# Optimization experiments

Measured on AMD Instinct MI355X. Metric: run time of the kernel, lower is better.

The kernel has to match this reference:

```python
import jax, jax.numpy as jnp
import numpy as np

B, NCAP, LV, LT, C = 64, 64, 197, 32, 512
NSP = LV - 1          # 196 spatial patches
NUM_KEEP = 98         # ceil(196 * sparse_ratio=0.5)
KEEPED = 49           # int(196 * aggr_ratio=0.5 * sparse_ratio=0.5)
HID = 102             # int(512 * dim_ratio=0.2)
LN_EPS = 1e-5


def _normalize(x):
    # torch F.normalize: x / max(||x||, 1e-12)
    return x / jnp.maximum(jnp.linalg.norm(x, axis=-1, keepdims=True), 1e-12)


def setup_inputs() -> dict:
    key = jax.random.key(0)
    ks = jax.random.split(key, 8)
    def rn(k, shape, s=0.02):
        return jax.random.normal(k, shape, jnp.float32) * s
    return {
        "img_embs": jax.random.normal(ks[0], (B, LV, C), jnp.float32),
        "cap_embs": jax.random.normal(ks[1], (NCAP, LT, C), jnp.float32),
        "cap_lens": jnp.full((NCAP,), LT, jnp.int32),
        "ln_gamma": jnp.ones((C,), jnp.float32),
        "ln_beta": jnp.zeros((C,), jnp.float32),
        "w1": rn(ks[2], (C, HID)), "b1": jnp.zeros((HID,), jnp.float32),
        "w2": rn(ks[3], (HID, KEEPED)), "b2": jnp.zeros((KEEPED,), jnp.float32),
        "aggr_scale": jnp.ones((1, 1, 1), jnp.float32),
        "wi2t": rn(ks[4], (C, C)), "bi2t": jnp.zeros((C,), jnp.float32),
        "wt2i": rn(ks[5], (C, C)), "bt2i": jnp.zeros((C,), jnp.float32),
        "temp": jnp.ones((1, 1, 1), jnp.float32),
    }


def _forward(img_embs, cap_embs, ln_gamma, ln_beta, w1, b1, w2, b2,
             aggr_scale, wi2t, bi2t, wt2i, bt2i, temp):
    img_norm = _normalize(img_embs)
    img_cls = img_embs[:, 0:1]              # [B,1,C]  has_cls_token branch
    img_sp = img_embs[:, 1:]                # [B,196,C]
    img_sp_norm = img_norm[:, 1:]
    # use_cls_as_glob_embd: global = normalized CLS (no grad)
    glo = jax.lax.stop_gradient(img_norm[:, 0:1])
    attn_x = jax.lax.stop_gradient(jnp.sum(glo * img_sp_norm, -1))  # [B,196]
    cap_norm = _normalize(cap_embs)
    bidx = jnp.arange(B)[:, None]

    def ln(x):
        m = x.mean(-1, keepdims=True)
        v = jnp.var(x, axis=-1, keepdims=True)
        return (x - m) / jnp.sqrt(v + LN_EPS) * ln_gamma + ln_beta

    def per_caption(cap_i, cap_i_norm):
        # cap_i, cap_i_norm: [LT, C]
        cap_glo = jax.lax.stop_gradient(_normalize(cap_i[0:1]))           # [1,C]
        attn_y = jax.lax.stop_gradient(jnp.sum(cap_glo[None] * img_sp_norm, -1))  # [B,196]
        # --- TokenSparse ---
        score = attn_x + attn_y
        order = jnp.argsort(-score, axis=1)                              # descending
        keep, nonkeep = order[:, :NUM_KEEP], order[:, NUM_KEEP:]
        sel = img_sp[bidx, keep]                                          # [B,98,C]
        non = img_sp[bidx, nonkeep]                                       # [B,98,C]
        non_score = jnp.take_along_axis(score, nonkeep, 1)
        extra = jnp.sum(non * jax.nn.softmax(non_score, axis=1)[..., None],
                        axis=1, keepdims=True)                            # [B,1,C]
        # --- TokenAggregation ---
        h = jax.nn.gelu(ln(sel) @ w1 + b1, approximate=False)             # [B,98,HID]
        w = jnp.swapaxes(h @ w2 + b2, 1, 2) * aggr_scale                  # [B,49,98]
        aggr = jax.nn.softmax(w, axis=2) @ sel                            # [B,49,C]
        # [cls, aggr, extra] -> [B,51,C], then normalize
        sel_tok = _normalize(jnp.concatenate([img_cls, aggr, extra], 1))
        Ls = sel_tok.shape[1]
        # --- 'attn' similarity ---
        cap_exp = jnp.broadcast_to(cap_i_norm[None], (B, LT, C))
        st = jnp.swapaxes(sel_tok, 1, 2)                                  # [B,C,51]
        c2i = jax.nn.leaky_relu(cap_exp @ st, negative_slope=0.1)         # [B,LT,51]
        a_i2t = jax.nn.softmax((cap_exp @ wi2t + bi2t) @ st / temp, axis=1)
        a_t2i = jax.nn.softmax((cap_exp @ wt2i + bt2i) @ st / temp, axis=2)
        return jnp.sum(a_i2t * c2i / Ls + a_t2i * c2i / LT, axis=(1, 2))  # [B]

    sims = jax.vmap(per_caption)(cap_embs, cap_norm)                      # [NCAP,B]
    return sims.T                                                         # [B,NCAP]


def reference(img_embs, cap_embs, cap_lens, ln_gamma, ln_beta, w1, b1, w2, b2,
              aggr_scale, wi2t, bi2t, wt2i, bt2i, temp):
    # cap_lens are all LT (static shapes); eval-mode output: similarity matrix.
    return _forward(img_embs, cap_embs, ln_gamma, ln_beta, w1, b1, w2, b2,
                    aggr_scale, wi2t, bi2t, wt2i, bt2i, temp)
```

## Files before the change

kernel.cpp:

```cpp
#include <hip/hip_runtime.h>
#include <math.h>

#define B     64
#define NCAP  64
#define LV    197
#define LT    32
#define C     512
#define NSP   196
#define NKEEP 98
#define HID   102
#define KEEPED 49

#define OFF_ATTNX   12608
#define OFF_WSMAT   25152
#define OFF_WT      639808
#define OFF_GLOT    1688384
#define OFF_ATTNYT  1721152
#define OFF_IMGT    14164800
#define OFF_QBB     17834816
#define OFF_QCAP    19407680

typedef unsigned int u32;
typedef unsigned short u16;
typedef __bf16 bf16x8 __attribute__((ext_vector_type(8)));
typedef float f32x4 __attribute__((ext_vector_type(4)));
typedef unsigned int uint4v __attribute__((ext_vector_type(4)));

__device__ __forceinline__ u16 f2bf(float f) {
    u32 u = __builtin_bit_cast(u32, f);
    return (u16)((u + 0x7FFFu + ((u >> 16) & 1u)) >> 16);
}
__device__ __forceinline__ bf16x8 ld_bf8(const u16* p) {
    uint4v v = *reinterpret_cast<const uint4v*>(p);
    return __builtin_bit_cast(bf16x8, v);
}

__device__ __forceinline__ float gelu_exact(float x) {
    return 0.5f * x * (1.f + erff(x * 0.70710678118654752f));
}

__global__ __launch_bounds__(256) void k_pre(const float* __restrict__ img,
                                             const float* __restrict__ cap,
                                             const float* __restrict__ wi2t,
                                             const float* __restrict__ wt2i,
                                             u16* __restrict__ imgTf,
                                             float* __restrict__ gloT,
                                             u16* __restrict__ Qbbf,
                                             u16* __restrict__ Qcap,
                                             u16* __restrict__ wT) {
    int idx = blockIdx.x, t = threadIdx.x;
    __shared__ __align__(16) u16 shb[64 * 224];

    if (idx < 512) {
        int b = idx >> 3, cg = idx & 7;
        for (int f = t; f < 64 * 27; f += 256) shb[(f / 27) * 224 + 197 + (f % 27)] = 0;
        int cc = t & 63;
        for (int sb = t >> 6; sb < 197; sb += 4) {
            float v = img[((size_t)b * LV + sb) * C + cg * 64 + cc];
            shb[cc * 224 + sb] = f2bf(v);
        }
        __syncthreads();
        const u32* Tu = (const u32*)shb;
        u32* outp = (u32*)imgTf + (size_t)b * 7 * 32 * 256;
        for (int f = t; f < 7 * 4 * 256; f += 256) {
            int ks = f >> 10, rem = f & 1023;
            int ctl = rem >> 8, g = rem & 255;
            int lane_o = g >> 2, j2 = g & 3;
            int quad_o = lane_o >> 4, l15_o = lane_o & 15;
            int ccl = ctl * 16 + l15_o;
            int s = ks * 32 + quad_o * 8 + 2 * j2;
            u32 v = Tu[ccl * 112 + (s >> 1)];
            outp[(size_t)(ks * 32 + cg * 4 + ctl) * 256 + g] = v;
        }
    } else if (idx < 1024) {
        int e = idx - 512, i = e >> 3, tg = e & 7;
        int lane = t & 63, wv = t >> 6;
        int tt = tg * 4 + wv;
        const float* row = cap + ((size_t)i * LT + tt) * C;
        float v[8]; float ss = 0.f;
#pragma unroll
        for (int q = 0; q < 8; ++q) { v[q] = row[lane + 64 * q]; ss += v[q] * v[q]; }
        for (int o = 32; o > 0; o >>= 1) ss += __shfl_down(ss, o);
        ss = __shfl(ss, 0);
        float inv = 1.f / fmaxf(sqrtf(ss), 1e-12f);
        u16* qrow = Qcap + ((size_t)i * 32 + tt) * C;
        int mi = tt >> 4, l15f = tt & 15;
        u16* qfb = Qbbf + (size_t)(i * 6 + mi) * 16 * 512;
#pragma unroll
        for (int q = 0; q < 8; ++q) {
            float n = v[q] * inv;
            u16 nb = f2bf(n);
            int c = lane + 64 * q;
            qrow[c] = nb;
            int ks = c >> 5, quadf = (c >> 3) & 3, jf = c & 7;
            qfb[(size_t)ks * 512 + (quadf * 16 + l15f) * 8 + jf] = nb;
            if (tt == 0) gloT[c * NCAP + i] = n;
        }
    } else {
        int e = idx - 1024;
        int mat = e >> 6, ty = e & 63, jg = ty >> 3, cg = ty & 7;
        const float* W = mat ? wt2i : wi2t;
        u16 (*tile)[65] = (u16(*)[65])shb;
        for (int f = t; f < 4096; f += 256) {
            int cc2 = f >> 6, jj = f & 63;
            tile[jj][cc2] = f2bf(W[(size_t)(cg * 64 + cc2) * 512 + jg * 64 + jj]);
        }
        __syncthreads();
        for (int f = t; f < 4096; f += 256) {
            int jj = f >> 6, cc2 = f & 63;
            wT[((size_t)mat * 512 + jg * 64 + jj) * 512 + cg * 64 + cc2] = tile[jj][cc2];
        }
    }
}

__global__ __launch_bounds__(512) void k_mid(const float* __restrict__ img,
                                             const u16* __restrict__ wT,
                                             const float* __restrict__ bi2t,
                                             const float* __restrict__ bt2i,
                                             const u16* __restrict__ Qcap,
                                             u16* __restrict__ Qbbf,
                                             const float* __restrict__ gamw,
                                             const float* __restrict__ betw,
                                             const float* __restrict__ w1,
                                             const float* __restrict__ b1,
                                             const float* __restrict__ w2,
                                             const float* __restrict__ b2,
                                             const float* __restrict__ scale_p,
                                             const float* __restrict__ gloT,
                                             float* __restrict__ attn_x,
                                             float* __restrict__ WsM,
                                             float* __restrict__ attn_yT) {
    int idx = blockIdx.x, t = threadIdx.x;
    __shared__ __align__(16) float shm[4960 + 16];

    if (idx < 256) {
        int i = idx & 63, p = idx >> 6;
        int lane = t & 63, wu = t >> 6;
        int l15 = lane & 15, quad = lane >> 4;
        int mat = wu >> 2;
        int miq = (wu >> 1) & 1;
        int nh  = wu & 1;
        int ni0 = p * 8 + nh * 4;
        const u16* Arow = Qcap + ((size_t)i * 32 + miq * 16 + l15) * 512;
        const u16* Wm   = wT + (size_t)mat * 512 * 512;
        f32x4 acc[4];
#pragma unroll
        for (int n = 0; n < 4; ++n) acc[n] = (f32x4){0.f, 0.f, 0.f, 0.f};
        bf16x8 A = ld_bf8(Arow + quad * 8);
        bf16x8 Bf[4];
#pragma unroll
        for (int n = 0; n < 4; ++n)
            Bf[n] = ld_bf8(Wm + (size_t)((ni0 + n) * 16 + l15) * 512 + quad * 8);
        for (int ks = 0; ks < 16; ++ks) {
            bf16x8 An; bf16x8 Bn[4];
            if (ks < 15) {
                An = ld_bf8(Arow + (ks + 1) * 32 + quad * 8);
#pragma unroll
                for (int n = 0; n < 4; ++n)
                    Bn[n] = ld_bf8(Wm + (size_t)((ni0 + n) * 16 + l15) * 512 + (ks + 1) * 32 + quad * 8);
            }
#pragma unroll
            for (int n = 0; n < 4; ++n)
                acc[n] = __builtin_amdgcn_mfma_f32_16x16x32_bf16(A, Bf[n], acc[n], 0, 0, 0);
            A = An;
#pragma unroll
            for (int n = 0; n < 4; ++n) Bf[n] = Bn[n];
        }
        const float* bias = mat ? bt2i : bi2t;
#pragma unroll
        for (int n = 0; n < 4; ++n) {
            int j = (ni0 + n) * 16 + l15;
            float bj = bias[j];
            int ksf = j >> 5, quadf = (j >> 3) & 3, jf = j & 7;
#pragma unroll
            for (int r = 0; r < 4; ++r) {
                int q = 32 + mat * 32 + miq * 16 + quad * 4 + r;
                int mi = q >> 4, l15f = q & 15;
                Qbbf[(size_t)((i * 6 + mi) * 16 + ksf) * 512 + (quadf * 16 + l15f) * 8 + jf]
                    = f2bf(acc[n][r] + bj);
            }
        }
    } else if (idx < 1856) {
        int e = idx - 256;
        int b = e / 25, sg = e - b * 25;
        int s0 = sg * 8;
        int R = NSP - s0; if (R > 8) R = 8;
        float (*lnr)[C]   = (float(*)[C])shm;
        float (*HH)[104]  = (float(*)[104])(shm + 4096);
        float (*redm)[4]  = (float(*)[4])(shm + 4928);

        int g = t >> 6, lane = t & 63;
        if (g < R) {
            const float* row = img + ((size_t)b * LV + 1 + s0 + g) * C;
            const float* cls = img + (size_t)b * LV * C;
            float sm = 0.f, ss = 0.f, dd = 0.f, sc = 0.f;
            for (int c = lane; c < C; c += 64) {
                float v = row[c];
                float cv = cls[c];
                sm += v; ss += v * v; dd += v * cv; sc += cv * cv;
                lnr[g][c] = v;
            }
            for (int o = 32; o > 0; o >>= 1) {
                sm += __shfl_down(sm, o);
                ss += __shfl_down(ss, o);
                dd += __shfl_down(dd, o);
                sc += __shfl_down(sc, o);
            }
            if (lane == 0) { redm[g][0] = sm; redm[g][1] = ss; redm[g][2] = dd; redm[g][3] = sc; }
        }
        __syncthreads();
        for (int f = t; f < R * C; f += 512) {
            int rr = f >> 9, c = f & 511;
            float mean = redm[rr][0] * (1.f / C);
            float var  = redm[rr][1] * (1.f / C) - mean * mean;
            float rstd = 1.f / sqrtf(var + 1e-5f);
            lnr[rr][c] = (lnr[rr][c] - mean) * rstd * gamw[c] + betw[c];
        }
        if (t < R) {
            float inv0 = 1.f / fmaxf(sqrtf(redm[t][3]), 1e-12f);
            float invs = 1.f / fmaxf(sqrtf(redm[t][1]), 1e-12f);
            attn_x[b * NSP + s0 + t] = redm[t][2] * inv0 * invs;
        }
        __syncthreads();
        if (t < 408) {
            int rr2 = t / 102;
            int j = t - rr2 * 102;
            int rw0 = rr2 * 2, rw1 = rr2 * 2 + 1;
            float a0 = b1[j], a1 = b1[j];
            for (int c = 0; c < C; ++c) {
                float wv = w1[c * HID + j];
                a0 += lnr[rw0][c] * wv;
                a1 += lnr[rw1][c] * wv;
            }
            if (rw0 < R) HH[rw0][j] = gelu_exact(a0);
            if (rw1 < R) HH[rw1][j] = gelu_exact(a1);
        }
        __syncthreads();
        float scale = scale_p[0];
        if (t < 392) {
            int k = t % 49, rh = t / 49;
            if (rh < R) {
                float a = b2[k];
                for (int h = 0; h < HID; ++h) a += HH[rh][h] * w2[h * 49 + k];
                WsM[((size_t)b * NSP + s0 + rh) * 49 + k] = a * scale;
            }
        }
    } else {
        int e = idx - 1856;
        int b = e / 25;
        int s0 = (e - b * 25) * 8;
        int R = NSP - s0; if (R > 8) R = 8;
        float (*xr)[C] = (float(*)[C])shm;
        float* rnorm = shm + 4096;

        for (int f = t; f < R * C; f += 512) {
            int rr = f >> 9, c = f & 511;
            xr[rr][c] = img[((size_t)b * LV + 1 + s0 + rr) * C + c];
        }
        __syncthreads();
        {
            int row = t >> 6, l = t & 63;
            if (row < R) {
                float ss = 0.f;
                for (int c = l; c < C; c += 64) { float v = xr[row][c]; ss += v * v; }
                for (int o = 32; o > 0; o >>= 1) ss += __shfl_down(ss, o);
                if (l == 0) rnorm[row] = 1.f / fmaxf(sqrtf(ss), 1e-12f);
            }
        }
        __syncthreads();
        for (int f = t; f < R * C; f += 512) {
            int rr = f >> 9, c = f & 511;
            xr[rr][c] *= rnorm[rr];
        }
        __syncthreads();
        int i = t & 63, w = t >> 6;
        if (w < R) {
            float a0 = 0.f;
            for (int c4 = 0; c4 < C / 4; ++c4) {
                float g0 = gloT[(c4 * 4 + 0) * NCAP + i];
                float g1 = gloT[(c4 * 4 + 1) * NCAP + i];
                float g2 = gloT[(c4 * 4 + 2) * NCAP + i];
                float g3 = gloT[(c4 * 4 + 3) * NCAP + i];
                float4 x0 = ((const float4*)xr[w])[c4];
                a0 += x0.x * g0 + x0.y * g1 + x0.z * g2 + x0.w * g3;
            }
            attn_yT[((size_t)b * NCAP + i) * NSP + s0 + w] = a0;
        }
    }
}

__global__ __launch_bounds__(512, 4) void k_main(const float* __restrict__ attn_x,
                                                 const float* __restrict__ attn_yT,
                                                 const float* __restrict__ WsM,
                                                 const u16* __restrict__ imgTf,
                                                 const u16* __restrict__ Qbbf,
                                                 const float* __restrict__ temp_p,
                                                 float* __restrict__ out) {
    int lin = blockIdx.x + NCAP * blockIdx.y;
    int b = (lin & 7) * 8 + ((lin >> 3) & 7);
    int i = lin >> 6;
    int t = threadIdx.x;
    int lane = t & 63, wu = t >> 6;
    int l15 = lane & 15, quad = lane >> 4;

    __shared__ __align__(16) u16 TnBuf[51 * 520];
    __shared__ float rowsq[8][64];
    __shared__ float invn[64];
    __shared__ float colM[51], colZ[51], rowM[32], rowZ[32], redw[8];
    __shared__ float scoreS[NSP];
    __shared__ int   keepL[NKEEP];
    __shared__ int   nonL[NKEEP];
    __shared__ float snon[NKEEP];
    __shared__ short rnkH[2][NSP];

    u16*   Pf   = TnBuf;
    float* ULDS = (float*)TnBuf;

    {
        uint4v* Pfv = (uint4v*)Pf;
        for (int f = t; f < 51 * 232 / 8; f += 512) Pfv[f] = (uint4v){0, 0, 0, 0};
    }
    if (t < NSP)
        scoreS[t] = attn_x[b * NSP + t] + attn_yT[((size_t)b * NCAP + i) * NSP + t];
    __syncthreads();
    if (t < 2 * NSP) {
        int half = (t >= NSP) ? 1 : 0;
        int s = t - half * NSP;
        float sv = scoreS[s];
        int u0 = half * 98, u1 = half ? NSP : 98;
        int r = 0;
        for (int u = u0; u < u1; ++u) {
            float o = scoreS[u];
            r += (o > sv) || (o == sv && u < s);
        }
        rnkH[half][s] = (short)r;
    }
    __syncthreads();
    if (t < NSP) {
        int r = rnkH[0][t] + rnkH[1][t];
        if (r < NKEEP) keepL[r] = t;
        else { nonL[r - NKEEP] = t; snon[r - NKEEP] = scoreS[t]; }
    }
    __syncthreads();
    if (t == 0) Pf[0] = 0x3F80;
    for (int f = t; f < NKEEP * KEEPED; f += 512) {
        int j = f / KEEPED, k = f - j * KEEPED;
        int s = keepL[j];
        Pf[(1 + k) * 232 + 1 + s] = f2bf(expf(WsM[((size_t)b * NSP + s) * KEEPED + k]));
    }
    if (t < NKEEP) Pf[50 * 232 + 1 + nonL[t]] = f2bf(expf(snon[t]));
    __syncthreads();

    const u16* imgTb = imgTf + (size_t)b * 7 * 32 * 512;
    f32x4 acc[4][4];
#pragma unroll
    for (int mi = 0; mi < 4; ++mi)
#pragma unroll
        for (int nj = 0; nj < 4; ++nj) acc[mi][nj] = (f32x4){0.f, 0.f, 0.f, 0.f};

    for (int ks = 0; ks < 7; ++ks) {
        bf16x8 Afr[4];
#pragma unroll
        for (int mi = 0; mi < 4; ++mi)
            Afr[mi] = ld_bf8(Pf + (mi * 16 + l15) * 232 + ks * 32 + quad * 8);
#pragma unroll
        for (int nj = 0; nj < 4; ++nj) {
            bf16x8 Bf = ld_bf8(imgTb + (size_t)(ks * 32 + wu * 4 + nj) * 512 + lane * 8);
#pragma unroll
            for (int mi = 0; mi < 4; ++mi)
                acc[mi][nj] = __builtin_amdgcn_mfma_f32_16x16x32_bf16(Afr[mi], Bf, acc[mi][nj], 0, 0, 0);
        }
    }

#pragma unroll
    for (int mi = 0; mi < 4; ++mi)
#pragma unroll
        for (int r = 0; r < 4; ++r) {
            float s = acc[mi][0][r] * acc[mi][0][r] + acc[mi][1][r] * acc[mi][1][r]
                    + acc[mi][2][r] * acc[mi][2][r] + acc[mi][3][r] * acc[mi][3][r];
            s += __shfl_down(s, 8); s += __shfl_down(s, 4);
            s += __shfl_down(s, 2); s += __shfl_down(s, 1);
            if (l15 == 0) rowsq[wu][mi * 16 + quad * 4 + r] = s;
        }
    __syncthreads();
    if (t < 64) {
        float s = 0.f;
#pragma unroll
        for (int w2 = 0; w2 < 8; ++w2) s += rowsq[w2][t];
        invn[t] = 1.f / fmaxf(sqrtf(s), 1e-12f);
    }
    __syncthreads();

#pragma unroll
    for (int mi = 0; mi < 4; ++mi)
#pragma unroll
        for (int r = 0; r < 4; ++r) {
            int row = mi * 16 + quad * 4 + r;
            if (row < 51) {
                float iv = invn[row];
#pragma unroll
                for (int nj = 0; nj < 4; ++nj)
                    TnBuf[row * 520 + (wu * 4 + nj) * 16 + l15] = f2bf(acc[mi][nj][r] * iv);
            }
        }
    __syncthreads();

    const u16* Qbf = Qbbf + (size_t)i * 6 * 16 * 512;
    f32x4 ua[3];
#pragma unroll
    for (int e = 0; e < 3; ++e) ua[e] = (f32x4){0.f, 0.f, 0.f, 0.f};

    if (wu < 6) {
        int mi = wu;
        const u16* Ar = Qbf + (size_t)mi * 16 * 512 + lane * 8;
        bf16x8 Af = ld_bf8(Ar);
        for (int ks = 0; ks < 16; ++ks) {
            bf16x8 An;
            if (ks < 15) An = ld_bf8(Ar + (ks + 1) * 512);
#pragma unroll
            for (int e = 0; e < 3; ++e) {
                bf16x8 Bf = ld_bf8(TnBuf + (e * 16 + l15) * 520 + ks * 32 + quad * 8);
                ua[e] = __builtin_amdgcn_mfma_f32_16x16x32_bf16(Af, Bf, ua[e], 0, 0, 0);
            }
            Af = An;
        }
    } else {
        int w2 = wu - 6;
        int rowB = 48 + l15; if (rowB > 50) rowB = 50;
        const u16* Ar0 = Qbf + (size_t)(3 * w2 + 0) * 16 * 512 + lane * 8;
        const u16* Ar1 = Qbf + (size_t)(3 * w2 + 1) * 16 * 512 + lane * 8;
        const u16* Ar2 = Qbf + (size_t)(3 * w2 + 2) * 16 * 512 + lane * 8;
        bf16x8 Af0 = ld_bf8(Ar0);
        bf16x8 Af1 = ld_bf8(Ar1);
        bf16x8 Af2 = ld_bf8(Ar2);
        for (int ks = 0; ks < 16; ++ks) {
            bf16x8 An0, An1, An2;
            if (ks < 15) {
                An0 = ld_bf8(Ar0 + (ks + 1) * 512);
                An1 = ld_bf8(Ar1 + (ks + 1) * 512);
                An2 = ld_bf8(Ar2 + (ks + 1) * 512);
            }
            bf16x8 Bf = ld_bf8(TnBuf + rowB * 520 + ks * 32 + quad * 8);
            ua[0] = __builtin_amdgcn_mfma_f32_16x16x32_bf16(Af0, Bf, ua[0], 0, 0, 0);
            ua[1] = __builtin_amdgcn_mfma_f32_16x16x32_bf16(Af1, Bf, ua[1], 0, 0, 0);
            ua[2] = __builtin_amdgcn_mfma_f32_16x16x32_bf16(Af2, Bf, ua[2], 0, 0, 0);
            Af0 = An0; Af1 = An1; Af2 = An2;
        }
    }
    __syncthreads();

    if (wu < 6) {
#pragma unroll
        for (int e = 0; e < 3; ++e) {
            int l = e * 16 + l15;
            int q0 = wu * 16 + quad * 4;
#pragma unroll
            for (int r = 0; r < 4; ++r) ULDS[(q0 + r) * 52 + l] = ua[e][r];
        }
    } else {
        int l = 48 + l15;
        if (l < 51) {
            int w2 = wu - 6;
#pragma unroll
            for (int e = 0; e < 3; ++e) {
                int q0 = (3 * w2 + e) * 16 + quad * 4;
#pragma unroll
                for (int r = 0; r < 4; ++r) ULDS[(q0 + r) * 52 + l] = ua[e][r];
            }
        }
    }
    __syncthreads();

    float invT = 1.f / temp_p[0];
    if (t < 408) {
        int l = t >> 3, sub = t & 7;
        float vbuf[4]; float mm = -1e30f;
#pragma unroll
        for (int q = 0; q < 4; ++q) {
            float v = ULDS[(32 + sub + 8 * q) * 52 + l] * invT;
            vbuf[q] = v;
            mm = fmaxf(mm, v);
        }
#pragma unroll
        for (int o = 1; o < 8; o <<= 1) mm = fmaxf(mm, __shfl_xor(mm, o, 8));
        float z = 0.f;
#pragma unroll
        for (int q = 0; q < 4; ++q) z += expf(vbuf[q] - mm);
#pragma unroll
        for (int o = 1; o < 8; o <<= 1) z += __shfl_xor(z, o, 8);
        if (sub == 0) { colM[l] = mm; colZ[l] = 1.f / z; }
    }
    if (t < 256) {
        int u = t >> 3, sub = t & 7;
        float vbuf[7]; int cnt = 0; float mm = -1e30f;
        for (int l = sub; l < 51; l += 8) {
            float v = ULDS[(64 + u) * 52 + l] * invT;
            vbuf[cnt++] = v;
            mm = fmaxf(mm, v);
        }
#pragma unroll
        for (int o = 1; o < 8; o <<= 1) mm = fmaxf(mm, __shfl_xor(mm, o, 8));
        float z = 0.f;
        for (int q = 0; q < cnt; ++q) z += expf(vbuf[q] - mm);
#pragma unroll
        for (int o = 1; o < 8; o <<= 1) z += __shfl_xor(z, o, 8);
        if (sub == 0) { rowM[u] = mm; rowZ[u] = 1.f / z; }
    }
    __syncthreads();

    float part = 0.f;
    for (int f = t; f < LT * 51; f += 512) {
        int u = f / 51, l = f - u * 51;
        float u0 = ULDS[u * 52 + l];
        float c2 = (u0 > 0.f) ? u0 : 0.1f * u0;
        float av = expf(ULDS[(32 + u) * 52 + l] * invT - colM[l]) * colZ[l];
        float bv = expf(ULDS[(64 + u) * 52 + l] * invT - rowM[u]) * rowZ[u];
        part += c2 * (av * (1.f / 51.f) + bv * (1.f / 32.f));
    }
    for (int o = 32; o > 0; o >>= 1) part += __shfl_down(part, o);
    if (lane == 0) redw[wu] = part;
    __syncthreads();
    if (t == 0) {
        float s = 0.f;
#pragma unroll
        for (int w2 = 0; w2 < 8; ++w2) s += redw[w2];
        out[b * NCAP + i] = s;
    }
}

extern "C" void kernel_launch(void* const* d_in, const int* in_sizes, int n_in,
                              void* d_out, int out_size, void* d_ws, size_t ws_size,
                              hipStream_t stream) {
    const float* img        = (const float*)d_in[0];
    const float* cap        = (const float*)d_in[1];
    const float* gamw       = (const float*)d_in[3];
    const float* betw       = (const float*)d_in[4];
    const float* w1         = (const float*)d_in[5];
    const float* b1         = (const float*)d_in[6];
    const float* w2         = (const float*)d_in[7];
    const float* b2         = (const float*)d_in[8];
    const float* aggr_scale = (const float*)d_in[9];
    const float* wi2t       = (const float*)d_in[10];
    const float* bi2t       = (const float*)d_in[11];
    const float* wt2i       = (const float*)d_in[12];
    const float* bt2i       = (const float*)d_in[13];
    const float* temp       = (const float*)d_in[14];
    float* out = (float*)d_out;

    float* ws      = (float*)d_ws;
    float* attn_x  = ws + OFF_ATTNX;
    float* WsM     = ws + OFF_WSMAT;
    u16*   wT      = (u16*)(ws + OFF_WT);
    float* gloT    = ws + OFF_GLOT;
    float* attn_yT = ws + OFF_ATTNYT;
    u16*   imgTf   = (u16*)(ws + OFF_IMGT);
    u16*   Qbbf    = (u16*)(ws + OFF_QBB);
    u16*   Qcap    = (u16*)(ws + OFF_QCAP);

    k_pre<<<dim3(1152), dim3(256), 0, stream>>>(img, cap, wi2t, wt2i, imgTf, gloT, Qbbf, Qcap, wT);
    k_mid<<<dim3(3456), dim3(512), 0, stream>>>(img, wT, bi2t, bt2i, Qcap, Qbbf, gamw, betw,
                                                w1, b1, w2, b2, aggr_scale, gloT,
                                                attn_x, WsM, attn_yT);
    k_main<<<dim3(NCAP, B), dim3(512), 0, stream>>>(attn_x, attn_yT, WsM, imgTf, Qbbf, temp, out);
}
```

Measured before the change: 427.4 us.

## Compute score-predictor MLP with bf16 MFMA using pre-swizzled weight fragments

The LayerNorm plus two-layer MLP that predicts aggregation weights moves from scalar fp32 FMA loops to bf16 MFMA 16x16x32 instructions. k_pre gains blocks that convert and swizzle w1 and w2 into MFMA fragment layout. Each k_mid block now handles 16 rows instead of 8, with LN results and hidden activations staged in shared memory as bf16. This removes the many scalar global weight reads in the MLP, at the cost of lower precision in the predicted weights and the softmax selection that follows.

```diff
diff --git a/kernel.cpp b/kernel.cpp
--- a/kernel.cpp
+++ b/kernel.cpp
@@ -19,6 +19,8 @@
 #define OFF_IMGT    14164800
 #define OFF_QBB     17834816
 #define OFF_QCAP    19407680
+#define OFF_W1TF    19931968
+#define OFF_W2TF    19960640
 
 typedef unsigned int u32;
 typedef unsigned short u16;
@@ -43,11 +45,15 @@
                                              const float* __restrict__ cap,
                                              const float* __restrict__ wi2t,
                                              const float* __restrict__ wt2i,
+                                             const float* __restrict__ w1,
+                                             const float* __restrict__ w2,
                                              u16* __restrict__ imgTf,
                                              float* __restrict__ gloT,
                                              u16* __restrict__ Qbbf,
                                              u16* __restrict__ Qcap,
-                                             u16* __restrict__ wT) {
+                                             u16* __restrict__ wT,
+                                             u16* __restrict__ w1Tf,
+                                             u16* __restrict__ w2Tf) {
     int idx = blockIdx.x, t = threadIdx.x;
     __shared__ __align__(16) u16 shb[64 * 224];
 
@@ -96,7 +102,7 @@
             qfb[(size_t)ks * 512 + (quadf * 16 + l15f) * 8 + jf] = nb;
             if (tt == 0) gloT[c * NCAP + i] = n;
         }
-    } else {
+    } else if (idx < 1152) {
         int e = idx - 1024;
         int mat = e >> 6, ty = e & 63, jg = ty >> 3, cg = ty & 7;
         const float* W = mat ? wt2i : wi2t;
@@ -110,6 +116,38 @@
             int jj = f >> 6, cc2 = f & 63;
             wT[((size_t)mat * 512 + jg * 64 + jj) * 512 + cg * 64 + cc2] = tile[jj][cc2];
         }
+    } else if (idx < 1159) {
+        int nt = idx - 1152;
+        u32* outp = (u32*)w1Tf + (size_t)nt * 16 * 256;
+        for (int f = t; f < 16 * 256; f += 256) {
+            int ks = f >> 8, g = f & 255;
+            int lane_o = g >> 2, j2 = g & 3;
+            int l15o = lane_o & 15, quado = lane_o >> 4;
+            int kk = ks * 32 + quado * 8 + 2 * j2;
+            int n = nt * 16 + l15o;
+            u32 lo = 0, hi = 0;
+            if (n < HID) {
+                lo = f2bf(w1[(size_t)kk * HID + n]);
+                hi = f2bf(w1[(size_t)(kk + 1) * HID + n]);
+            }
+            outp[ks * 256 + g] = lo | (hi << 16);
+        }
+    } else {
+        u32* outp = (u32*)w2Tf;
+        for (int f = t; f < 16 * 256; f += 256) {
+            int tile = f >> 8, g = f & 255;
+            int nt2 = tile >> 2, ks2 = tile & 3;
+            int lane_o = g >> 2, j2 = g & 3;
+            int l15o = lane_o & 15, quado = lane_o >> 4;
+            int kk0 = ks2 * 32 + quado * 8 + 2 * j2;
+            int n = nt2 * 16 + l15o;
+            u32 lo = 0, hi = 0;
+            if (n < KEEPED) {
+                if (kk0 < HID)     lo = f2bf(w2[(size_t)kk0 * KEEPED + n]);
+                if (kk0 + 1 < HID) hi = f2bf(w2[(size_t)(kk0 + 1) * KEEPED + n]);
+            }
+            outp[tile * 256 + g] = lo | (hi << 16);
+        }
     }
 }
 
@@ -119,11 +157,11 @@
                                              const float* __restrict__ bt2i,
                                              const u16* __restrict__ Qcap,
                                              u16* __restrict__ Qbbf,
+                                             const u16* __restrict__ w1Tf,
+                                             const u16* __restrict__ w2Tf,
                                              const float* __restrict__ gamw,
                                              const float* __restrict__ betw,
-                                             const float* __restrict__ w1,
                                              const float* __restrict__ b1,
-                                             const float* __restrict__ w2,
                                              const float* __restrict__ b2,
                                              const float* __restrict__ scale_p,
                                              const float* __restrict__ gloT,
@@ -131,7 +169,7 @@
                                              float* __restrict__ WsM,
                                              float* __restrict__ attn_yT) {
     int idx = blockIdx.x, t = threadIdx.x;
-    __shared__ __align__(16) float shm[4960 + 16];
+    __shared__ __align__(16) u16 shu[16 * 520 + 16 * 136];
 
     if (idx < 256) {
         int i = idx & 63, p = idx >> 6;
@@ -180,78 +218,110 @@
                     = f2bf(acc[n][r] + bj);
             }
         }
-    } else if (idx < 1856) {
+    } else if (idx < 1088) {
         int e = idx - 256;
-        int b = e / 25, sg = e - b * 25;
-        int s0 = sg * 8;
-        int R = NSP - s0; if (R > 8) R = 8;
-        float (*lnr)[C]   = (float(*)[C])shm;
-        float (*HH)[104]  = (float(*)[104])(shm + 4096);
-        float (*redm)[4]  = (float(*)[4])(shm + 4928);
-
-        int g = t >> 6, lane = t & 63;
-        if (g < R) {
-            const float* row = img + ((size_t)b * LV + 1 + s0 + g) * C;
-            const float* cls = img + (size_t)b * LV * C;
-            float sm = 0.f, ss = 0.f, dd = 0.f, sc = 0.f;
-            for (int c = lane; c < C; c += 64) {
-                float v = row[c];
+        int b = e / 13, sg = e - b * 13;
+        int s0 = sg * 16;
+        u16* LNb = shu;
+        u16* Hb  = shu + 16 * 520;
+        int lane = t & 63, wu = t >> 6;
+        int l15 = lane & 15, quad = lane >> 4;
+
+        {
+            int rr0 = 2 * wu, rr1 = 2 * wu + 1;
+            int sA = s0 + rr0, sB = s0 + rr1;
+            int sAc = sA < NSP ? sA : NSP - 1;
+            int sBc = sB < NSP ? sB : NSP - 1;
+            const float* rowA = img + ((size_t)b * LV + 1 + sAc) * C;
+            const float* rowB = img + ((size_t)b * LV + 1 + sBc) * C;
+            const float* cls  = img + (size_t)b * LV * C;
+            float v0[8], v1[8];
+            float sm0 = 0, ss0 = 0, dd0 = 0, sm1 = 0, ss1 = 0, dd1 = 0, sc = 0;
+#pragma unroll
+            for (int q = 0; q < 8; ++q) {
+                int c = lane + 64 * q;
                 float cv = cls[c];
-                sm += v; ss += v * v; dd += v * cv; sc += cv * cv;
-                lnr[g][c] = v;
+                v0[q] = rowA[c]; v1[q] = rowB[c];
+                sm0 += v0[q]; ss0 += v0[q] * v0[q]; dd0 += v0[q] * cv;
+                sm1 += v1[q]; ss1 += v1[q] * v1[q]; dd1 += v1[q] * cv;
+                sc  += cv * cv;
             }
             for (int o = 32; o > 0; o >>= 1) {
-                sm += __shfl_down(sm, o);
-                ss += __shfl_down(ss, o);
-                dd += __shfl_down(dd, o);
-                sc += __shfl_down(sc, o);
-            }
-            if (lane == 0) { redm[g][0] = sm; redm[g][1] = ss; redm[g][2] = dd; redm[g][3] = sc; }
+                sm0 += __shfl_down(sm0, o); ss0 += __shfl_down(ss0, o); dd0 += __shfl_down(dd0, o);
+                sm1 += __shfl_down(sm1, o); ss1 += __shfl_down(ss1, o); dd1 += __shfl_down(dd1, o);
+                sc  += __shfl_down(sc, o);
+            }
+            sm0 = __shfl(sm0, 0); ss0 = __shfl(ss0, 0);
+            sm1 = __shfl(sm1, 0); ss1 = __shfl(ss1, 0);
+            float mean0 = sm0 * (1.f / C);
+            float rstd0 = 1.f / sqrtf(ss0 * (1.f / C) - mean0 * mean0 + 1e-5f);
+            float mean1 = sm1 * (1.f / C);
+            float rstd1 = 1.f / sqrtf(ss1 * (1.f / C) - mean1 * mean1 + 1e-5f);
+            if (lane == 0) {
+                float inv0 = 1.f / fmaxf(sqrtf(sc), 1e-12f);
+                if (sA < NSP) attn_x[b * NSP + sA] = dd0 * inv0 * (1.f / fmaxf(sqrtf(ss0), 1e-12f));
+                if (sB < NSP) attn_x[b * NSP + sB] = dd1 * inv0 * (1.f / fmaxf(sqrtf(ss1), 1e-12f));
+            }
+#pragma unroll
+            for (int q = 0; q < 8; ++q) {
+                int c = lane + 64 * q;
+                float g = gamw[c], be = betw[c];
+                LNb[rr0 * 520 + c] = f2bf((v0[q] - mean0) * rstd0 * g + be);
+                LNb[rr1 * 520 + c] = f2bf((v1[q] - mean1) * rstd1 * g + be);
+            }
         }
         __syncthreads();
-        for (int f = t; f < R * C; f += 512) {
-            int rr = f >> 9, c = f & 511;
-            float mean = redm[rr][0] * (1.f / C);
-            float var  = redm[rr][1] * (1.f / C) - mean * mean;
-            float rstd = 1.f / sqrtf(var + 1e-5f);
-            lnr[rr][c] = (lnr[rr][c] - mean) * rstd * gamw[c] + betw[c];
-        }
-        if (t < R) {
-            float inv0 = 1.f / fmaxf(sqrtf(redm[t][3]), 1e-12f);
-            float invs = 1.f / fmaxf(sqrtf(redm[t][1]), 1e-12f);
-            attn_x[b * NSP + s0 + t] = redm[t][2] * inv0 * invs;
+        if (wu < 7) {
+            const u16* W1b = w1Tf + (size_t)wu * 16 * 512;
+            f32x4 h4 = (f32x4){0.f, 0.f, 0.f, 0.f};
+            for (int ks = 0; ks < 16; ++ks) {
+                bf16x8 A = ld_bf8(LNb + l15 * 520 + ks * 32 + quad * 8);
+                bf16x8 Bv = ld_bf8(W1b + ks * 512 + lane * 8);
+                h4 = __builtin_amdgcn_mfma_f32_16x16x32_bf16(A, Bv, h4, 0, 0, 0);
+            }
+            int col = wu * 16 + l15;
+            if (col < HID) {
+                float bb = b1[col];
+#pragma unroll
+                for (int r = 0; r < 4; ++r)
+                    Hb[(quad * 4 + r) * 136 + col] = f2bf(gelu_exact(h4[r] + bb));
+            } else {
+#pragma unroll
+                for (int r = 0; r < 4; ++r) Hb[(quad * 4 + r) * 136 + col] = 0;
+            }
+        } else {
+            for (int f = lane; f < 16 * 24; f += 64) {
+                int row = f / 24, cc = 112 + f % 24;
+                Hb[row * 136 + cc] = 0;
+            }
         }
         __syncthreads();
-        if (t < 408) {
-            int rr2 = t / 102;
-            int j = t - rr2 * 102;
-            int rw0 = rr2 * 2, rw1 = rr2 * 2 + 1;
-            float a0 = b1[j], a1 = b1[j];
-            for (int c = 0; c < C; ++c) {
-                float wv = w1[c * HID + j];
-                a0 += lnr[rw0][c] * wv;
-                a1 += lnr[rw1][c] * wv;
-            }
-            if (rw0 < R) HH[rw0][j] = gelu_exact(a0);
-            if (rw1 < R) HH[rw1][j] = gelu_exact(a1);
-        }
-        __syncthreads();
-        float scale = scale_p[0];
-        if (t < 392) {
-            int k = t % 49, rh = t / 49;
-            if (rh < R) {
-                float a = b2[k];
-                for (int h = 0; h < HID; ++h) a += HH[rh][h] * w2[h * 49 + k];
-                WsM[((size_t)b * NSP + s0 + rh) * 49 + k] = a * scale;
+        if (wu < 4) {
+            const u16* W2b = w2Tf + (size_t)wu * 4 * 512;
+            f32x4 a2 = (f32x4){0.f, 0.f, 0.f, 0.f};
+            for (int ks2 = 0; ks2 < 4; ++ks2) {
+                bf16x8 A2 = ld_bf8(Hb + l15 * 136 + ks2 * 32 + quad * 8);
+                bf16x8 B2 = ld_bf8(W2b + ks2 * 512 + lane * 8);
+                a2 = __builtin_amdgcn_mfma_f32_16x16x32_bf16(A2, B2, a2, 0, 0, 0);
+            }
+            int k = wu * 16 + l15;
+            if (k < KEEPED) {
+                float scale = scale_p[0], bk = b2[k];
+#pragma unroll
+                for (int r = 0; r < 4; ++r) {
+                    int row = quad * 4 + r;
+                    if (s0 + row < NSP)
+                        WsM[((size_t)b * NSP + s0 + row) * 49 + k] = (a2[r] + bk) * scale;
+                }
             }
         }
     } else {
-        int e = idx - 1856;
+        int e = idx - 1088;
         int b = e / 25;
         int s0 = (e - b * 25) * 8;
         int R = NSP - s0; if (R > 8) R = 8;
-        float (*xr)[C] = (float(*)[C])shm;
-        float* rnorm = shm + 4096;
+        float (*xr)[C] = (float(*)[C])shu;
+        float* rnorm = (float*)shu + 4096;
 
         for (int f = t; f < R * C; f += 512) {
             int rr = f >> 9, c = f & 511;
@@ -556,10 +626,13 @@
     u16*   imgTf   = (u16*)(ws + OFF_IMGT);
     u16*   Qbbf    = (u16*)(ws + OFF_QBB);
     u16*   Qcap    = (u16*)(ws + OFF_QCAP);
-
-    k_pre<<<dim3(1152), dim3(256), 0, stream>>>(img, cap, wi2t, wt2i, imgTf, gloT, Qbbf, Qcap, wT);
-    k_mid<<<dim3(3456), dim3(512), 0, stream>>>(img, wT, bi2t, bt2i, Qcap, Qbbf, gamw, betw,
-                                                w1, b1, w2, b2, aggr_scale, gloT,
-                                                attn_x, WsM, attn_yT);
+    u16*   w1Tf    = (u16*)(ws + OFF_W1TF);
+    u16*   w2Tf    = (u16*)(ws + OFF_W2TF);
+
+    k_pre<<<dim3(1160), dim3(256), 0, stream>>>(img, cap, wi2t, wt2i, w1, w2,
+                                                imgTf, gloT, Qbbf, Qcap, wT, w1Tf, w2Tf);
+    k_mid<<<dim3(2688), dim3(512), 0, stream>>>(img, wT, bi2t, bt2i, Qcap, Qbbf,
+                                                w1Tf, w2Tf, gamw, betw, b1, b2, aggr_scale,
+                                                gloT, attn_x, WsM, attn_yT);
     k_main<<<dim3(NCAP, B), dim3(512), 0, stream>>>(attn_x, attn_yT, WsM, imgTf, Qbbf, temp, out);
 }
```

Result: faster. 364.0 us (-14.8%).
